# Optimization experiments

Hardware: AMD Instinct MI355X
Metric: run time of the kernel (lower is better)

The kernel has to match this reference:

```python
import jax, jax.numpy as jnp
import numpy as np
from jax.ops import segment_sum

N_NODES = 50000
N_EDGES = 600000
HIDDEN = 128
N_FEAT = 128
N_CLASSES = 10
N_GRAPHS = 128


def setup_inputs() -> dict:
    key = jax.random.key(0)
    ks = jax.random.split(key, 16)
    x = jax.random.normal(ks[0], (N_NODES, N_FEAT), dtype=jnp.float32)
    edge_index = jax.random.randint(ks[1], (2, N_EDGES), 0, N_NODES, dtype=jnp.int64)
    batch = jnp.sort(jax.random.randint(ks[2], (N_NODES,), 0, N_GRAPHS, dtype=jnp.int64))
    def lin_init(k, fan_in, fan_out):
        s = 1.0 / np.sqrt(fan_in)
        return jax.random.uniform(k, (fan_in, fan_out), jnp.float32, -s, s)
    params = {
        'W1': lin_init(ks[3], N_FEAT, HIDDEN), 'b1': jnp.zeros((HIDDEN,), jnp.float32),
        'W2': lin_init(ks[4], HIDDEN, HIDDEN), 'b2': jnp.zeros((HIDDEN,), jnp.float32),
        'W3': lin_init(ks[5], HIDDEN, HIDDEN), 'b3': jnp.zeros((HIDDEN,), jnp.float32),
        'W4': lin_init(ks[6], HIDDEN, HIDDEN), 'b4': jnp.zeros((HIDDEN,), jnp.float32),
        'W5': lin_init(ks[7], HIDDEN, HIDDEN), 'b5': jnp.zeros((HIDDEN,), jnp.float32),
        'Wfc': lin_init(ks[8], HIDDEN, HIDDEN), 'bfc': jnp.zeros((HIDDEN,), jnp.float32),
        'Wlin': lin_init(ks[9], HIDDEN, N_CLASSES), 'blin': jnp.zeros((N_CLASSES,), jnp.float32),
    }
    return dict(x=x, edge_index=edge_index, batch=batch, **params)


def _gcn_edges(edge_index, n_nodes):
    # PyG GCNConv default: add self-loops, symmetric deg^-1/2 normalization.
    loop = jnp.arange(n_nodes, dtype=edge_index.dtype)
    row = jnp.concatenate([edge_index[0], loop])  # source (messages gathered from)
    col = jnp.concatenate([edge_index[1], loop])  # target (scatter-add into)
    deg = segment_sum(jnp.ones_like(col, dtype=jnp.float32), col, num_segments=n_nodes)
    dinv = jnp.where(deg > 0, jax.lax.rsqrt(deg), 0.0)
    norm = dinv[row] * dinv[col]  # [E+N]
    return row, col, norm


def _gcn_conv(x, W, b, row, col, norm, n_nodes):
    h = x @ W  # [N, out]
    agg = segment_sum(h[row] * norm[:, None], col, num_segments=n_nodes)
    return agg + b


def reference(x, edge_index, batch, W1, b1, W2, b2, W3, b3, W4, b4, W5, b5, Wfc, bfc, Wlin, blin):
    n = x.shape[0]
    row, col, norm = _gcn_edges(edge_index, n)
    h = jax.nn.relu(_gcn_conv(x, W1, b1, row, col, norm, n))
    h = jax.nn.relu(_gcn_conv(h, W2, b2, row, col, norm, n))
    h = jax.nn.relu(_gcn_conv(h, W3, b3, row, col, norm, n))
    h = jax.nn.relu(_gcn_conv(h, W4, b4, row, col, norm, n))
    h = jax.nn.relu(_gcn_conv(h, W5, b5, row, col, norm, n))
    h = jax.nn.relu(h @ Wfc + bfc)
    # global_mean_pool over batch ids
    sums = segment_sum(h, batch, num_segments=N_GRAPHS)
    cnts = segment_sum(jnp.ones((n,), h.dtype), batch, num_segments=N_GRAPHS)
    pooled = sums / jnp.maximum(cnts, 1.0)[:, None]  # [G, H]
    embeddings = pooled
    # dropout p=0.5 is identity in eval mode
    logits = pooled @ Wlin + blin  # [G, C]
    return logits, jnp.squeeze(embeddings)
```

## Files before the change

kernel.cpp:

```cpp
#include <hip/hip_runtime.h>

typedef __attribute__((ext_vector_type(8))) short short8;
typedef __attribute__((ext_vector_type(4))) float floatx4;
typedef __attribute__((ext_vector_type(4))) unsigned uintx4;
typedef __attribute__((ext_vector_type(8))) _Float16 half8;

static __device__ __forceinline__ unsigned short f2bf(float f) {
    unsigned u = __float_as_uint(f);
    u += 0x7fff + ((u >> 16) & 1);
    return (unsigned short)(u >> 16);
}
static __device__ __forceinline__ float bf2f(unsigned short h) {
    return __uint_as_float((unsigned)h << 16);
}


__global__ void count_kernel(const int* __restrict__ ei, int* degi, int E) {
    int e = blockIdx.x * 256 + threadIdx.x;
    if (e < E) atomicAdd(&degi[ei[E + e]], 1);
}

__global__ __launch_bounds__(256) void scan_bsum_kernel(const int* __restrict__ degi,
                                                        float* __restrict__ dinv,
                                                        int* bsum, int n) {
    int tid = threadIdx.x;
    int i = blockIdx.x * 256 + tid;
    int d = (i < n) ? degi[i] : 0;
    if (i < n) dinv[i] = rsqrtf((float)(d + 1));
    int v = d;
    #pragma unroll
    for (int off = 32; off > 0; off >>= 1) v += __shfl_down(v, off);
    __shared__ int ws[4];
    if ((tid & 63) == 0) ws[tid >> 6] = v;
    __syncthreads();
    if (tid == 0) bsum[blockIdx.x] = ws[0] + ws[1] + ws[2] + ws[3];
}

__global__ __launch_bounds__(256) void scan_emit_kernel(const int* __restrict__ degi,
                                                        const int* __restrict__ bsum,
                                                        int* rp, int* cursor, int n, int nb) {
    int tid = threadIdx.x;
    int bid = blockIdx.x;
    int contrib = 0;
    for (int t = tid; t < bid; t += 256) contrib += bsum[t];
    int cr = contrib;
    #pragma unroll
    for (int off = 32; off > 0; off >>= 1) cr += __shfl_down(cr, off);
    __shared__ int wr[4];
    __shared__ int s_boff;
    if ((tid & 63) == 0) wr[tid >> 6] = cr;
    __syncthreads();
    if (tid == 0) s_boff = wr[0] + wr[1] + wr[2] + wr[3];
    __syncthreads();

    int i = bid * 256 + tid;
    int v = (i < n) ? degi[i] : 0;
    int lane = tid & 63, wid = tid >> 6;
    int x = v;
    #pragma unroll
    for (int off = 1; off < 64; off <<= 1) {
        int y = __shfl_up(x, off);
        if (lane >= off) x += y;
    }
    __shared__ int ws[4];
    if (lane == 63) ws[wid] = x;
    __syncthreads();
    if (tid == 0) { int a = 0; for (int j = 0; j < 4; ++j) { int t = ws[j]; ws[j] = a; a += t; } }
    __syncthreads();
    int excl = x - v + ws[wid] + s_boff;
    if (i < n) { rp[i] = excl; cursor[i] = excl; }
    if (i == n - 1) rp[n] = excl + v;
}

__global__ void fill_kernel(const int* __restrict__ ei, int* cursor,
                            int* __restrict__ csr, int E) {
    int e = blockIdx.x * 256 + threadIdx.x;
    if (e >= E) return;
    int r = ei[e], c = ei[E + e];
    int pos = atomicAdd(&cursor[c], 1);
    csr[pos] = r;
}


__global__ void packw_kernel(const float* w0, const float* w1, const float* w2,
                             const float* w3, const float* w4, const float* w5,
                             unsigned short* __restrict__ hi, unsigned short* __restrict__ lo) {
    int l = blockIdx.y;
    const float* W = (l == 0) ? w0 : (l == 1) ? w1 : (l == 2) ? w2
                   : (l == 3) ? w3 : (l == 4) ? w4 : w5;
    int idx = blockIdx.x * 256 + threadIdx.x;
    int k = idx >> 7, nn = idx & 127;
    float v = W[k * 128 + nn];
    unsigned short h = f2bf(v);
    unsigned short ls = f2bf(v - bf2f(h));
    hi[l * 16384 + nn * 128 + k] = h;
    lo[l * 16384 + nn * 128 + k] = ls;
}


#define WLDS_STRIDE 260

static __device__ __forceinline__ void stage_w(const unsigned short* __restrict__ Wth,
                                               const unsigned short* __restrict__ Wtl,
                                               unsigned short* Wlds, int tid) {
    #pragma unroll
    for (int it = 0; it < 8; ++it) {
        int c = it * 512 + tid;
        int row = c >> 5, piece = c & 31;
        const unsigned short* src = (piece < 16)
            ? (Wth + (size_t)row * 128 + piece * 8)
            : (Wtl + (size_t)row * 128 + (piece - 16) * 8);
        int dst = row * WLDS_STRIDE + ((piece < 16) ? piece * 8 : 128 + (piece - 16) * 8);
        *(short8*)&Wlds[dst] = *(const short8*)src;
    }
}

static __device__ __forceinline__ void split_h8(half8 a, short8& ah, short8& al) {
    #pragma unroll
    for (int j = 0; j < 8; ++j) {
        float fv = (float)a[j];
        unsigned u = __float_as_uint(fv);
        float lo = fv - __uint_as_float(u & 0xFFFF0000u);
        ah[j] = (short)(u >> 16);
        al[j] = (short)(__float_as_uint(lo) >> 16);
    }
}

__global__ __launch_bounds__(512, 4) void gemm_kernel(const _Float16* __restrict__ A,
                                                      const unsigned short* __restrict__ Wth,
                                                      const unsigned short* __restrict__ Wtl,
                                                      const float* __restrict__ dinv,
                                                      void* __restrict__ C, int n, int outf) {
    __shared__ unsigned short Wlds[128 * WLDS_STRIDE];
    int tid = threadIdx.x;
    int wave = tid >> 6, lane = tid & 63;
    int m = lane & 15, quad = lane >> 4;
    int row0 = blockIdx.x * 128 + wave * 16;
    int arow = row0 + m; if (arow > n - 1) arow = n - 1;
    size_t n32 = (size_t)n * 32;
    const _Float16* abase = A + (size_t)arow * 32 + quad * 8;

    half8 pa[4];
    #pragma unroll
    for (int kc = 0; kc < 4; ++kc) pa[kc] = *(const half8*)(abase + (size_t)kc * n32);

    stage_w(Wth, Wtl, Wlds, tid);

    floatx4 acc[8];
    #pragma unroll
    for (int ct = 0; ct < 8; ++ct) acc[ct] = (floatx4){0.f, 0.f, 0.f, 0.f};
    __syncthreads();

    #pragma unroll
    for (int kc = 0; kc < 4; ++kc) {
        short8 ah, al;
        split_h8(pa[kc], ah, al);
        #pragma unroll
        for (int ct = 0; ct < 8; ++ct) {
            int base = (ct * 16 + m) * WLDS_STRIDE + kc * 32 + quad * 8;
            short8 wh = *(const short8*)&Wlds[base];
            short8 wl = *(const short8*)&Wlds[base + 128];
            acc[ct] = __builtin_amdgcn_mfma_f32_16x16x32_bf16(ah, wl, acc[ct], 0, 0, 0);
            acc[ct] = __builtin_amdgcn_mfma_f32_16x16x32_bf16(al, wh, acc[ct], 0, 0, 0);
            acc[ct] = __builtin_amdgcn_mfma_f32_16x16x32_bf16(ah, wh, acc[ct], 0, 0, 0);
        }
    }

    float dv[4];
    #pragma unroll
    for (int r = 0; r < 4; ++r) dv[r] = dinv[min(row0 + quad * 4 + r, n - 1)];

    #pragma unroll
    for (int ct = 0; ct < 8; ++ct) {
        #pragma unroll
        for (int r = 0; r < 4; ++r) {
            int row = row0 + quad * 4 + r;
            if (row < n) {
                if (outf) {
                    ((float*)C)[(size_t)row * 128 + ct * 16 + m] = acc[ct][r];
                } else {
                    ((_Float16*)C)[(size_t)(ct >> 1) * n32 + (size_t)row * 32
                                   + (ct & 1) * 16 + m] = (_Float16)(acc[ct][r] * dv[r]);
                }
            }
        }
    }
}

__global__ __launch_bounds__(512, 4) void gemm0_kernel(const float* __restrict__ X,
                                                       const unsigned short* __restrict__ Wth,
                                                       const unsigned short* __restrict__ Wtl,
                                                       const float* __restrict__ dinv,
                                                       _Float16* __restrict__ C, int n) {
    __shared__ unsigned short Wlds[128 * WLDS_STRIDE];
    int tid = threadIdx.x;
    int wave = tid >> 6, lane = tid & 63;
    int m = lane & 15, quad = lane >> 4;
    int row0 = blockIdx.x * 128 + wave * 16;
    int arow = row0 + m; if (arow > n - 1) arow = n - 1;
    size_t n32 = (size_t)n * 32;
    const float* aptr = X + (size_t)arow * 128 + quad * 8;

    floatx4 pf0[4], pf1[4];
    #pragma unroll
    for (int kc = 0; kc < 4; ++kc) {
        pf0[kc] = *(const floatx4*)(aptr + kc * 32);
        pf1[kc] = *(const floatx4*)(aptr + kc * 32 + 4);
    }

    stage_w(Wth, Wtl, Wlds, tid);

    floatx4 acc[8];
    #pragma unroll
    for (int ct = 0; ct < 8; ++ct) acc[ct] = (floatx4){0.f, 0.f, 0.f, 0.f};
    __syncthreads();

    #pragma unroll
    for (int kc = 0; kc < 4; ++kc) {
        short8 ah, al;
        #pragma unroll
        for (int j = 0; j < 8; ++j) {
            float fv = (j < 4) ? pf0[kc][j] : pf1[kc][j - 4];
            unsigned short h = f2bf(fv);
            ah[j] = (short)h;
            al[j] = (short)f2bf(fv - bf2f(h));
        }
        #pragma unroll
        for (int ct = 0; ct < 8; ++ct) {
            int base = (ct * 16 + m) * WLDS_STRIDE + kc * 32 + quad * 8;
            short8 wh = *(const short8*)&Wlds[base];
            short8 wl = *(const short8*)&Wlds[base + 128];
            acc[ct] = __builtin_amdgcn_mfma_f32_16x16x32_bf16(ah, wl, acc[ct], 0, 0, 0);
            acc[ct] = __builtin_amdgcn_mfma_f32_16x16x32_bf16(al, wh, acc[ct], 0, 0, 0);
            acc[ct] = __builtin_amdgcn_mfma_f32_16x16x32_bf16(ah, wh, acc[ct], 0, 0, 0);
        }
    }

    float dv[4];
    #pragma unroll
    for (int r = 0; r < 4; ++r) dv[r] = dinv[min(row0 + quad * 4 + r, n - 1)];

    #pragma unroll
    for (int ct = 0; ct < 8; ++ct) {
        #pragma unroll
        for (int r = 0; r < 4; ++r) {
            int row = row0 + quad * 4 + r;
            if (row < n)
                C[(size_t)(ct >> 1) * n32 + (size_t)row * 32 + (ct & 1) * 16 + m] =
                    (_Float16)(acc[ct][r] * dv[r]);
        }
    }
}


__global__ __launch_bounds__(256) void agg_kernel(const _Float16* __restrict__ t,
                                                  const float* __restrict__ bias,
                                                  const int* __restrict__ rp,
                                                  const int* __restrict__ csr,
                                                  const float* __restrict__ dinv,
                                                  _Float16* __restrict__ outp, int n, int nh) {
    int s = blockIdx.x & 7;
    int chunk = s & 3;
    int half = s >> 2;
    int nb = blockIdx.x >> 3;
    int group = threadIdx.x >> 2;
    int lane4 = threadIdx.x & 3;
    int j = half * nh + nb * 64 + group;
    int jend = half ? n : nh;
    if (j >= jend) return;
    size_t n32 = (size_t)n * 32;
    const _Float16* tc = t + (size_t)chunk * n32;
    int c8 = lane4 * 8;
    int p0 = rp[j], p1 = rp[j + 1];

    float dj = dinv[j];
    half8 vs = *(const half8*)&tc[(size_t)j * 32 + c8];

    float acc[8];
    #pragma unroll
    for (int k = 0; k < 8; ++k) acc[k] = (float)vs[k];

    int p = p0;
    for (; p + 8 <= p1; p += 8) {
        int e[8];
        #pragma unroll
        for (int i = 0; i < 8; ++i) e[i] = csr[p + i];
        half8 v[8];
        #pragma unroll
        for (int i = 0; i < 8; ++i)
            v[i] = *(const half8*)&tc[(size_t)e[i] * 32 + c8];
        #pragma unroll
        for (int i = 0; i < 8; ++i) {
            #pragma unroll
            for (int k = 0; k < 8; ++k) acc[k] += (float)v[i][k];
        }
    }
    if (p < p1) {
        int lim = p1 - 1;
        int e[8];
        #pragma unroll
        for (int i = 0; i < 8; ++i) e[i] = csr[min(p + i, lim)];
        float msk[8];
        #pragma unroll
        for (int i = 0; i < 8; ++i) msk[i] = (p + i < p1) ? 1.f : 0.f;
        half8 v[8];
        #pragma unroll
        for (int i = 0; i < 8; ++i)
            v[i] = *(const half8*)&tc[(size_t)e[i] * 32 + c8];
        #pragma unroll
        for (int i = 0; i < 8; ++i) {
            #pragma unroll
            for (int k = 0; k < 8; ++k) acc[k] += msk[i] * (float)v[i][k];
        }
    }

    int cbase = chunk * 32 + c8;
    float4 b0 = *(const float4*)&bias[cbase];
    float4 b1 = *(const float4*)&bias[cbase + 4];
    float bb[8] = {b0.x, b0.y, b0.z, b0.w, b1.x, b1.y, b1.z, b1.w};
    half8 hv;
    #pragma unroll
    for (int k = 0; k < 8; ++k) hv[k] = (_Float16)fmaxf(fmaf(dj, acc[k], bb[k]), 0.f);

    *(half8*)&outp[(size_t)chunk * n32 + (size_t)j * 32 + c8] = hv;
}


__global__ __launch_bounds__(256) void pool_kernel(const float* __restrict__ t,
                                                   const float* __restrict__ bfc,
                                                   const int* __restrict__ batch,
                                                   const float* __restrict__ Wlin,
                                                   const float* __restrict__ blin,
                                                   float* __restrict__ out, int n) {
    int g = blockIdx.x;
    int tid = threadIdx.x;
    int lo = 0, hi = n;
    while (lo < hi) { int m = (lo + hi) >> 1; if (batch[m] < g) lo = m + 1; else hi = m; }
    int start = lo;
    lo = start; hi = n;
    while (lo < hi) { int m = (lo + hi) >> 1; if (batch[m] < g + 1) lo = m + 1; else hi = m; }
    int end = lo;

    int lane = tid & 31, sub = tid >> 5;
    int c4 = lane * 4;
    float4 bv = *(const float4*)&bfc[c4];
    float sx = 0.f, sy = 0.f, sz = 0.f, sw = 0.f;
    for (int j = start + sub; j < end; j += 8) {
        float4 v = *(const float4*)&t[(size_t)j * 128 + c4];
        sx += fmaxf(v.x + bv.x, 0.f);
        sy += fmaxf(v.y + bv.y, 0.f);
        sz += fmaxf(v.z + bv.z, 0.f);
        sw += fmaxf(v.w + bv.w, 0.f);
    }
    __shared__ float red[8][128];
    red[sub][c4] = sx; red[sub][c4 + 1] = sy; red[sub][c4 + 2] = sz; red[sub][c4 + 3] = sw;
    __syncthreads();
    __shared__ float pooled[128];
    if (tid < 128) {
        float s = 0.f;
        #pragma unroll
        for (int k = 0; k < 8; ++k) s += red[k][tid];
        float pv = s / fmaxf((float)(end - start), 1.f);
        pooled[tid] = pv;
        out[1280 + g * 128 + tid] = pv;
    }
    __syncthreads();
    if (tid < 10) {
        float a = blin[tid];
        for (int k = 0; k < 128; ++k) a += pooled[k] * Wlin[k * 10 + tid];
        out[g * 10 + tid] = a;
    }
}


extern "C" void kernel_launch(void* const* d_in, const int* in_sizes, int n_in,
                              void* d_out, int out_size, void* d_ws, size_t ws_size,
                              hipStream_t stream) {
    const float* x     = (const float*)d_in[0];
    const int*   ei    = (const int*)d_in[1];
    const int*   batch = (const int*)d_in[2];
    const float* Wl[6] = {(const float*)d_in[3], (const float*)d_in[5], (const float*)d_in[7],
                          (const float*)d_in[9], (const float*)d_in[11], (const float*)d_in[13]};
    const float* bl[6] = {(const float*)d_in[4], (const float*)d_in[6], (const float*)d_in[8],
                          (const float*)d_in[10], (const float*)d_in[12], (const float*)d_in[14]};
    const float* Wlin = (const float*)d_in[15];
    const float* blin = (const float*)d_in[16];

    const int N = in_sizes[2];
    const int E = in_sizes[1] / 2;
    (void)n_in; (void)out_size; (void)ws_size;

    char* p = (char*)d_ws;
    auto carve = [&](size_t bytes) { void* r = (void*)p; p += (bytes + 255) & ~(size_t)255; return r; };
    _Float16*       tA     = (_Float16*)carve((size_t)N * 128 * 2);
    _Float16*       tB     = (_Float16*)carve((size_t)N * 128 * 2);
    float*          tf     = (float*)carve((size_t)N * 128 * 4);
    int*            degi   = (int*)carve((size_t)N * 4);
    float*          dinv   = (float*)carve((size_t)N * 4);
    int*            rp     = (int*)carve((size_t)(N + 1) * 4);
    int*            cursor = (int*)carve((size_t)N * 4);
    int*            csr    = (int*)carve((size_t)E * 4);
    int*            bsum   = (int*)carve(256 * 4);
    unsigned short* wth    = (unsigned short*)carve(6 * 16384 * 2);
    unsigned short* wtl    = (unsigned short*)carve(6 * 16384 * 2);

    int gN = (N + 255) / 256;
    hipMemsetAsync(degi, 0, (size_t)N * 4, stream);
    count_kernel<<<(E + 255) / 256, 256, 0, stream>>>(ei, degi, E);
    scan_bsum_kernel<<<gN, 256, 0, stream>>>(degi, dinv, bsum, N);
    scan_emit_kernel<<<gN, 256, 0, stream>>>(degi, bsum, rp, cursor, N, gN);
    fill_kernel<<<(E + 255) / 256, 256, 0, stream>>>(ei, cursor, csr, E);
    packw_kernel<<<dim3(64, 6), 256, 0, stream>>>(Wl[0], Wl[1], Wl[2], Wl[3], Wl[4], Wl[5],
                                                  wth, wtl);

    int NH = (N + 1) / 2;
    int gGemm = (N + 127) / 128;
    int gAgg  = 8 * ((NH + 63) / 64);
    gemm0_kernel<<<gGemm, 512, 0, stream>>>(x, wth, wtl, dinv, tA, N);
    agg_kernel<<<gAgg, 256, 0, stream>>>(tA, bl[0], rp, csr, dinv, tB, N, NH);
    for (int l = 1; l < 5; ++l) {
        gemm_kernel<<<gGemm, 512, 0, stream>>>(tB, wth + l * 16384, wtl + l * 16384,
                                               dinv, (void*)tA, N, 0);
        agg_kernel<<<gAgg, 256, 0, stream>>>(tA, bl[l], rp, csr, dinv, tB, N, NH);
    }
    gemm_kernel<<<gGemm, 512, 0, stream>>>(tB, wth + 5 * 16384, wtl + 5 * 16384,
                                           dinv, (void*)tf, N, 1);
    pool_kernel<<<128, 256, 0, stream>>>(tf, bl[5], batch, Wlin, blin, (float*)d_out, N);
}
```

Measured before the change: 396.0 us.

## Fuse GCN layer GEMMs and aggregations into one cooperative persistent kernel

Replaces the sequence of eleven separate GEMM and aggregation launches with a single cooperative kernel of 512 blocks, using grid-wide syncs between stages. Aggregation work is grid-strided across the persistent blocks, and the GEMM tiles run on the first blocks. The goal is to remove per-launch overhead and inter-kernel gaps. In exchange it pays grid.sync costs, and the large LDS footprint caps how many blocks fit per CU, so the gather-heavy aggregation runs at lower occupancy than before. The original multi-kernel path is kept as a fallback if the cooperative launch fails.

```diff
diff --git a/kernel.cpp b/kernel.cpp
--- a/kernel.cpp
+++ b/kernel.cpp
@@ -1,8 +1,10 @@
 #include <hip/hip_runtime.h>
+#include <hip/hip_cooperative_groups.h>
+
+namespace cg = cooperative_groups;
 
 typedef __attribute__((ext_vector_type(8))) short short8;
 typedef __attribute__((ext_vector_type(4))) float floatx4;
-typedef __attribute__((ext_vector_type(4))) unsigned uintx4;
 typedef __attribute__((ext_vector_type(8))) _Float16 half8;
 
 static __device__ __forceinline__ unsigned short f2bf(float f) {
@@ -99,6 +101,8 @@
 
 
 #define WLDS_STRIDE 260
+#define COOP_GRID 512
+#define AGG_STRIDE ((COOP_GRID / 8) * 128)
 
 static __device__ __forceinline__ void stage_w(const unsigned short* __restrict__ Wth,
                                                const unsigned short* __restrict__ Wtl,
@@ -126,16 +130,17 @@
     }
 }
 
-__global__ __launch_bounds__(512, 4) void gemm_kernel(const _Float16* __restrict__ A,
-                                                      const unsigned short* __restrict__ Wth,
-                                                      const unsigned short* __restrict__ Wtl,
-                                                      const float* __restrict__ dinv,
-                                                      void* __restrict__ C, int n, int outf) {
-    __shared__ unsigned short Wlds[128 * WLDS_STRIDE];
-    int tid = threadIdx.x;
+static __device__ __forceinline__ void gemm_body_f16(const _Float16* __restrict__ A,
+                                                     const unsigned short* __restrict__ Wth,
+                                                     const unsigned short* __restrict__ Wtl,
+                                                     const float* __restrict__ dinv,
+                                                     _Float16* __restrict__ C16,
+                                                     float* __restrict__ C32, int outf,
+                                                     unsigned short* Wlds, int tid, int bid,
+                                                     int n) {
     int wave = tid >> 6, lane = tid & 63;
     int m = lane & 15, quad = lane >> 4;
-    int row0 = blockIdx.x * 128 + wave * 16;
+    int row0 = bid * 128 + wave * 16;
     int arow = row0 + m; if (arow > n - 1) arow = n - 1;
     size_t n32 = (size_t)n * 32;
     const _Float16* abase = A + (size_t)arow * 32 + quad * 8;
@@ -177,26 +182,26 @@
             int row = row0 + quad * 4 + r;
             if (row < n) {
                 if (outf) {
-                    ((float*)C)[(size_t)row * 128 + ct * 16 + m] = acc[ct][r];
+                    C32[(size_t)row * 128 + ct * 16 + m] = acc[ct][r];
                 } else {
-                    ((_Float16*)C)[(size_t)(ct >> 1) * n32 + (size_t)row * 32
-                                   + (ct & 1) * 16 + m] = (_Float16)(acc[ct][r] * dv[r]);
+                    C16[(size_t)(ct >> 1) * n32 + (size_t)row * 32 + (ct & 1) * 16 + m] =
+                        (_Float16)(acc[ct][r] * dv[r]);
                 }
             }
         }
     }
 }
 
-__global__ __launch_bounds__(512, 4) void gemm0_kernel(const float* __restrict__ X,
-                                                       const unsigned short* __restrict__ Wth,
-                                                       const unsigned short* __restrict__ Wtl,
-                                                       const float* __restrict__ dinv,
-                                                       _Float16* __restrict__ C, int n) {
-    __shared__ unsigned short Wlds[128 * WLDS_STRIDE];
-    int tid = threadIdx.x;
+static __device__ __forceinline__ void gemm_body_f32(const float* __restrict__ X,
+                                                     const unsigned short* __restrict__ Wth,
+                                                     const unsigned short* __restrict__ Wtl,
+                                                     const float* __restrict__ dinv,
+                                                     _Float16* __restrict__ C,
+                                                     unsigned short* Wlds, int tid, int bid,
+                                                     int n) {
     int wave = tid >> 6, lane = tid & 63;
     int m = lane & 15, quad = lane >> 4;
-    int row0 = blockIdx.x * 128 + wave * 16;
+    int row0 = bid * 128 + wave * 16;
     int arow = row0 + m; if (arow > n - 1) arow = n - 1;
     size_t n32 = (size_t)n * 32;
     const float* aptr = X + (size_t)arow * 128 + quad * 8;
@@ -252,6 +257,130 @@
     }
 }
 
+static __device__ __forceinline__ void agg_node(const _Float16* __restrict__ tc,
+                                                const float* __restrict__ bias,
+                                                const int* __restrict__ rp,
+                                                const int* __restrict__ csr,
+                                                const float* __restrict__ dinv,
+                                                _Float16* __restrict__ outp,
+                                                int j, int chunk, int c8, size_t n32) {
+    int p0 = rp[j], p1 = rp[j + 1];
+    float dj = dinv[j];
+    half8 vs = *(const half8*)&tc[(size_t)j * 32 + c8];
+
+    float acc[8];
+    #pragma unroll
+    for (int k = 0; k < 8; ++k) acc[k] = (float)vs[k];
+
+    int p = p0;
+    for (; p + 8 <= p1; p += 8) {
+        int e[8];
+        #pragma unroll
+        for (int i = 0; i < 8; ++i) e[i] = csr[p + i];
+        half8 v[8];
+        #pragma unroll
+        for (int i = 0; i < 8; ++i)
+            v[i] = *(const half8*)&tc[(size_t)e[i] * 32 + c8];
+        #pragma unroll
+        for (int i = 0; i < 8; ++i) {
+            #pragma unroll
+            for (int k = 0; k < 8; ++k) acc[k] += (float)v[i][k];
+        }
+    }
+    if (p < p1) {
+        int lim = p1 - 1;
+        int e[8];
+        #pragma unroll
+        for (int i = 0; i < 8; ++i) e[i] = csr[min(p + i, lim)];
+        float msk[8];
+        #pragma unroll
+        for (int i = 0; i < 8; ++i) msk[i] = (p + i < p1) ? 1.f : 0.f;
+        half8 v[8];
+        #pragma unroll
+        for (int i = 0; i < 8; ++i)
+            v[i] = *(const half8*)&tc[(size_t)e[i] * 32 + c8];
+        #pragma unroll
+        for (int i = 0; i < 8; ++i) {
+            #pragma unroll
+            for (int k = 0; k < 8; ++k) acc[k] += msk[i] * (float)v[i][k];
+        }
+    }
+
+    int cbase = chunk * 32 + c8;
+    float4 b0 = *(const float4*)&bias[cbase];
+    float4 b1 = *(const float4*)&bias[cbase + 4];
+    float bb[8] = {b0.x, b0.y, b0.z, b0.w, b1.x, b1.y, b1.z, b1.w};
+    half8 hv;
+    #pragma unroll
+    for (int k = 0; k < 8; ++k) hv[k] = (_Float16)fmaxf(fmaf(dj, acc[k], bb[k]), 0.f);
+
+    *(half8*)&outp[(size_t)chunk * n32 + (size_t)j * 32 + c8] = hv;
+}
+
+
+__global__ __launch_bounds__(512, 4) void net_kernel(
+    const float* __restrict__ X,
+    const unsigned short* __restrict__ wth, const unsigned short* __restrict__ wtl,
+    const float* __restrict__ b0, const float* __restrict__ b1,
+    const float* __restrict__ b2, const float* __restrict__ b3,
+    const float* __restrict__ b4,
+    const float* __restrict__ dinv, const int* __restrict__ rp,
+    const int* __restrict__ csr,
+    _Float16* __restrict__ tA, _Float16* __restrict__ tB,
+    float* __restrict__ tf, int n, int nh) {
+    cg::grid_group grid = cg::this_grid();
+    __shared__ unsigned short Wlds[128 * WLDS_STRIDE];
+    const int tid = threadIdx.x;
+    const int bid = blockIdx.x;
+    const int gGemm = (n + 127) >> 7;
+    const size_t n32 = (size_t)n * 32;
+
+    const int s = bid & 7;
+    const int chunk = s & 3;
+    const int half = s >> 2;
+    const int group0 = ((bid >> 3) << 7) + (tid >> 2);
+    const int c8 = (tid & 3) * 8;
+    const int cnt = half ? (n - nh) : nh;
+
+    if (bid < gGemm)
+        gemm_body_f32(X, wth, wtl, dinv, tA, Wlds, tid, bid, n);
+    grid.sync();
+
+    for (int l = 1; l <= 5; ++l) {
+        const float* bias = (l == 1) ? b0 : (l == 2) ? b1 : (l == 3) ? b2
+                          : (l == 4) ? b3 : b4;
+        const _Float16* tc = tA + (size_t)chunk * n32;
+        for (int ln = group0; ln < cnt; ln += AGG_STRIDE)
+            agg_node(tc, bias, rp, csr, dinv, tB, half * nh + ln, chunk, c8, n32);
+        grid.sync();
+
+        if (bid < gGemm)
+            gemm_body_f16(tB, wth + l * 16384, wtl + l * 16384, dinv,
+                          tA, tf, (l == 5) ? 1 : 0, Wlds, tid, bid, n);
+        if (l < 5) grid.sync();
+    }
+}
+
+
+__global__ __launch_bounds__(512, 4) void gemm_kernel(const _Float16* __restrict__ A,
+                                                      const unsigned short* __restrict__ Wth,
+                                                      const unsigned short* __restrict__ Wtl,
+                                                      const float* __restrict__ dinv,
+                                                      _Float16* __restrict__ C16,
+                                                      float* __restrict__ C32,
+                                                      int n, int outf) {
+    __shared__ unsigned short Wlds[128 * WLDS_STRIDE];
+    gemm_body_f16(A, Wth, Wtl, dinv, C16, C32, outf, Wlds, threadIdx.x, blockIdx.x, n);
+}
+
+__global__ __launch_bounds__(512, 4) void gemm0_kernel(const float* __restrict__ X,
+                                                       const unsigned short* __restrict__ Wth,
+                                                       const unsigned short* __restrict__ Wtl,
+                                                       const float* __restrict__ dinv,
+                                                       _Float16* __restrict__ C, int n) {
+    __shared__ unsigned short Wlds[128 * WLDS_STRIDE];
+    gemm_body_f32(X, Wth, Wtl, dinv, C, Wlds, threadIdx.x, blockIdx.x, n);
+}
 
 __global__ __launch_bounds__(256) void agg_kernel(const _Float16* __restrict__ t,
                                                   const float* __restrict__ bias,
@@ -269,60 +398,7 @@
     int jend = half ? n : nh;
     if (j >= jend) return;
     size_t n32 = (size_t)n * 32;
-    const _Float16* tc = t + (size_t)chunk * n32;
-    int c8 = lane4 * 8;
-    int p0 = rp[j], p1 = rp[j + 1];
-
-    float dj = dinv[j];
-    half8 vs = *(const half8*)&tc[(size_t)j * 32 + c8];
-
-    float acc[8];
-    #pragma unroll
-    for (int k = 0; k < 8; ++k) acc[k] = (float)vs[k];
-
-    int p = p0;
-    for (; p + 8 <= p1; p += 8) {
-        int e[8];
-        #pragma unroll
-        for (int i = 0; i < 8; ++i) e[i] = csr[p + i];
-        half8 v[8];
-        #pragma unroll
-        for (int i = 0; i < 8; ++i)
-            v[i] = *(const half8*)&tc[(size_t)e[i] * 32 + c8];
-        #pragma unroll
-        for (int i = 0; i < 8; ++i) {
-            #pragma unroll
-            for (int k = 0; k < 8; ++k) acc[k] += (float)v[i][k];
-        }
-    }
-    if (p < p1) {
-        int lim = p1 - 1;
-        int e[8];
-        #pragma unroll
-        for (int i = 0; i < 8; ++i) e[i] = csr[min(p + i, lim)];
-        float msk[8];
-        #pragma unroll
-        for (int i = 0; i < 8; ++i) msk[i] = (p + i < p1) ? 1.f : 0.f;
-        half8 v[8];
-        #pragma unroll
-        for (int i = 0; i < 8; ++i)
-            v[i] = *(const half8*)&tc[(size_t)e[i] * 32 + c8];
-        #pragma unroll
-        for (int i = 0; i < 8; ++i) {
-            #pragma unroll
-            for (int k = 0; k < 8; ++k) acc[k] += msk[i] * (float)v[i][k];
-        }
-    }
-
-    int cbase = chunk * 32 + c8;
-    float4 b0 = *(const float4*)&bias[cbase];
-    float4 b1 = *(const float4*)&bias[cbase + 4];
-    float bb[8] = {b0.x, b0.y, b0.z, b0.w, b1.x, b1.y, b1.z, b1.w};
-    half8 hv;
-    #pragma unroll
-    for (int k = 0; k < 8; ++k) hv[k] = (_Float16)fmaxf(fmaf(dj, acc[k], bb[k]), 0.f);
-
-    *(half8*)&outp[(size_t)chunk * n32 + (size_t)j * 32 + c8] = hv;
+    agg_node(t + (size_t)chunk * n32, bias, rp, csr, dinv, outp, j, chunk, lane4 * 8, n32);
 }
 
 
@@ -414,16 +490,34 @@
                                                   wth, wtl);
 
     int NH = (N + 1) / 2;
-    int gGemm = (N + 127) / 128;
-    int gAgg  = 8 * ((NH + 63) / 64);
-    gemm0_kernel<<<gGemm, 512, 0, stream>>>(x, wth, wtl, dinv, tA, N);
-    agg_kernel<<<gAgg, 256, 0, stream>>>(tA, bl[0], rp, csr, dinv, tB, N, NH);
-    for (int l = 1; l < 5; ++l) {
-        gemm_kernel<<<gGemm, 512, 0, stream>>>(tB, wth + l * 16384, wtl + l * 16384,
-                                               dinv, (void*)tA, N, 0);
-        agg_kernel<<<gAgg, 256, 0, stream>>>(tA, bl[l], rp, csr, dinv, tB, N, NH);
-    }
-    gemm_kernel<<<gGemm, 512, 0, stream>>>(tB, wth + 5 * 16384, wtl + 5 * 16384,
-                                           dinv, (void*)tf, N, 1);
+
+    {
+        const float* xx = x;
+        const unsigned short* wthv = wth; const unsigned short* wtlv = wtl;
+        const float* bb0 = bl[0]; const float* bb1 = bl[1]; const float* bb2 = bl[2];
+        const float* bb3 = bl[3]; const float* bb4 = bl[4];
+        const float* dinvv = dinv; const int* rpv = rp; const int* csrv = csr;
+        _Float16* tAv = tA; _Float16* tBv = tB; float* tfv = tf;
+        int Nv = N, NHv = NH;
+        void* args[] = {&xx, &wthv, &wtlv, &bb0, &bb1, &bb2, &bb3, &bb4,
+                        &dinvv, &rpv, &csrv, &tAv, &tBv, &tfv, &Nv, &NHv};
+        hipError_t ce = hipLaunchCooperativeKernel((void*)net_kernel,
+                                                   dim3(COOP_GRID), dim3(512),
+                                                   args, 0, stream);
+        if (ce != hipSuccess) {
+            int gGemm = (N + 127) / 128;
+            int gAgg  = 8 * ((NH + 63) / 64);
+            gemm0_kernel<<<gGemm, 512, 0, stream>>>(x, wth, wtl, dinv, tA, N);
+            agg_kernel<<<gAgg, 256, 0, stream>>>(tA, bl[0], rp, csr, dinv, tB, N, NH);
+            for (int l = 1; l < 5; ++l) {
+                gemm_kernel<<<gGemm, 512, 0, stream>>>(tB, wth + l * 16384, wtl + l * 16384,
+                                                       dinv, tA, (float*)nullptr, N, 0);
+                agg_kernel<<<gAgg, 256, 0, stream>>>(tA, bl[l], rp, csr, dinv, tB, N, NH);
+            }
+            gemm_kernel<<<gGemm, 512, 0, stream>>>(tB, wth + 5 * 16384, wtl + 5 * 16384,
+                                                   dinv, (_Float16*)nullptr, tf, N, 1);
+        }
+    }
+
     pool_kernel<<<128, 256, 0, stream>>>(tf, bl[5], batch, Wlin, blin, (float*)d_out, N);
 }
```

Result: slower. 1.201 ms (+203.4%).

## Switch intermediate features from chunked column layout to row-major with LDS-transposed stores

Applied to the files above, without the earlier changes.

The fp16 intermediate features move from a layout split into four 32-column chunks to a plain row-major [N,128] layout. The GEMM epilogues now stage results through LDS and write each row with contiguous 16-byte stores. The aggregation kernel uses 16 threads per node, so each neighbour gather reads one full 256-byte row instead of four separate 64-byte pieces spread across chunk-specialized blocks. The cost is an extra LDS round trip and two barriers in the GEMM, and each aggregation block now reads the whole row rather than a chunk, which changes L2 reuse behaviour.

```diff
diff --git a/kernel.cpp b/kernel.cpp
--- a/kernel.cpp
+++ b/kernel.cpp
@@ -2,7 +2,6 @@
 
 typedef __attribute__((ext_vector_type(8))) short short8;
 typedef __attribute__((ext_vector_type(4))) float floatx4;
-typedef __attribute__((ext_vector_type(4))) unsigned uintx4;
 typedef __attribute__((ext_vector_type(8))) _Float16 half8;
 
 static __device__ __forceinline__ unsigned short f2bf(float f) {
@@ -99,6 +98,7 @@
 
 
 #define WLDS_STRIDE 260
+#define TR_STRIDE 132
 
 static __device__ __forceinline__ void stage_w(const unsigned short* __restrict__ Wth,
                                                const unsigned short* __restrict__ Wtl,
@@ -137,12 +137,11 @@
     int m = lane & 15, quad = lane >> 4;
     int row0 = blockIdx.x * 128 + wave * 16;
     int arow = row0 + m; if (arow > n - 1) arow = n - 1;
-    size_t n32 = (size_t)n * 32;
-    const _Float16* abase = A + (size_t)arow * 32 + quad * 8;
+    const _Float16* abase = A + (size_t)arow * 128 + quad * 8;
 
     half8 pa[4];
     #pragma unroll
-    for (int kc = 0; kc < 4; ++kc) pa[kc] = *(const half8*)(abase + (size_t)kc * n32);
+    for (int kc = 0; kc < 4; ++kc) pa[kc] = *(const half8*)(abase + kc * 32);
 
     stage_w(Wth, Wtl, Wlds, tid);
 
@@ -170,19 +169,36 @@
     #pragma unroll
     for (int r = 0; r < 4; ++r) dv[r] = dinv[min(row0 + quad * 4 + r, n - 1)];
 
-    #pragma unroll
-    for (int ct = 0; ct < 8; ++ct) {
-        #pragma unroll
-        for (int r = 0; r < 4; ++r) {
-            int row = row0 + quad * 4 + r;
-            if (row < n) {
-                if (outf) {
-                    ((float*)C)[(size_t)row * 128 + ct * 16 + m] = acc[ct][r];
-                } else {
-                    ((_Float16*)C)[(size_t)(ct >> 1) * n32 + (size_t)row * 32
-                                   + (ct & 1) * 16 + m] = (_Float16)(acc[ct][r] * dv[r]);
-                }
+    if (outf) {
+        #pragma unroll
+        for (int ct = 0; ct < 8; ++ct) {
+            #pragma unroll
+            for (int r = 0; r < 4; ++r) {
+                int row = row0 + quad * 4 + r;
+                if (row < n) ((float*)C)[(size_t)row * 128 + ct * 16 + m] = acc[ct][r];
             }
+        }
+    } else {
+        __syncthreads();
+        _Float16* tr = (_Float16*)Wlds;
+        #pragma unroll
+        for (int ct = 0; ct < 8; ++ct) {
+            #pragma unroll
+            for (int r = 0; r < 4; ++r) {
+                int rl = wave * 16 + quad * 4 + r;
+                tr[rl * TR_STRIDE + ct * 16 + m] = (_Float16)(acc[ct][r] * dv[r]);
+            }
+        }
+        __syncthreads();
+        int rl2 = tid >> 2;
+        int seg = tid & 3;
+        int grow = blockIdx.x * 128 + rl2;
+        if (grow < n) {
+            _Float16* dst = (_Float16*)C + (size_t)grow * 128 + seg * 32;
+            const _Float16* src = tr + rl2 * TR_STRIDE + seg * 32;
+            #pragma unroll
+            for (int k = 0; k < 4; ++k)
+                *(half8*)(dst + k * 8) = *(const half8*)(src + k * 8);
         }
     }
 }
@@ -198,7 +214,6 @@
     int m = lane & 15, quad = lane >> 4;
     int row0 = blockIdx.x * 128 + wave * 16;
     int arow = row0 + m; if (arow > n - 1) arow = n - 1;
-    size_t n32 = (size_t)n * 32;
     const float* aptr = X + (size_t)arow * 128 + quad * 8;
 
     floatx4 pf0[4], pf1[4];
@@ -240,15 +255,26 @@
     #pragma unroll
     for (int r = 0; r < 4; ++r) dv[r] = dinv[min(row0 + quad * 4 + r, n - 1)];
 
+    __syncthreads();
+    _Float16* tr = (_Float16*)Wlds;
     #pragma unroll
     for (int ct = 0; ct < 8; ++ct) {
         #pragma unroll
         for (int r = 0; r < 4; ++r) {
-            int row = row0 + quad * 4 + r;
-            if (row < n)
-                C[(size_t)(ct >> 1) * n32 + (size_t)row * 32 + (ct & 1) * 16 + m] =
-                    (_Float16)(acc[ct][r] * dv[r]);
-        }
+            int rl = wave * 16 + quad * 4 + r;
+            tr[rl * TR_STRIDE + ct * 16 + m] = (_Float16)(acc[ct][r] * dv[r]);
+        }
+    }
+    __syncthreads();
+    int rl2 = tid >> 2;
+    int seg = tid & 3;
+    int grow = blockIdx.x * 128 + rl2;
+    if (grow < n) {
+        _Float16* dst = C + (size_t)grow * 128 + seg * 32;
+        const _Float16* src = tr + rl2 * TR_STRIDE + seg * 32;
+        #pragma unroll
+        for (int k = 0; k < 4; ++k)
+            *(half8*)(dst + k * 8) = *(const half8*)(src + k * 8);
     }
 }
 
@@ -258,24 +284,14 @@
                                                   const int* __restrict__ rp,
                                                   const int* __restrict__ csr,
                                                   const float* __restrict__ dinv,
-                                                  _Float16* __restrict__ outp, int n, int nh) {
-    int s = blockIdx.x & 7;
-    int chunk = s & 3;
-    int half = s >> 2;
-    int nb = blockIdx.x >> 3;
-    int group = threadIdx.x >> 2;
-    int lane4 = threadIdx.x & 3;
-    int j = half * nh + nb * 64 + group;
-    int jend = half ? n : nh;
-    if (j >= jend) return;
-    size_t n32 = (size_t)n * 32;
-    const _Float16* tc = t + (size_t)chunk * n32;
-    int c8 = lane4 * 8;
+                                                  _Float16* __restrict__ outp, int n) {
+    int j = blockIdx.x * 16 + (threadIdx.x >> 4);
+    if (j >= n) return;
+    int c8 = (threadIdx.x & 15) * 8;
     int p0 = rp[j], p1 = rp[j + 1];
-
     float dj = dinv[j];
-    half8 vs = *(const half8*)&tc[(size_t)j * 32 + c8];
-
+
+    half8 vs = *(const half8*)&t[(size_t)j * 128 + c8];
     float acc[8];
     #pragma unroll
     for (int k = 0; k < 8; ++k) acc[k] = (float)vs[k];
@@ -288,7 +304,7 @@
         half8 v[8];
         #pragma unroll
         for (int i = 0; i < 8; ++i)
-            v[i] = *(const half8*)&tc[(size_t)e[i] * 32 + c8];
+            v[i] = *(const half8*)&t[(size_t)e[i] * 128 + c8];
         #pragma unroll
         for (int i = 0; i < 8; ++i) {
             #pragma unroll
@@ -306,7 +322,7 @@
         half8 v[8];
         #pragma unroll
         for (int i = 0; i < 8; ++i)
-            v[i] = *(const half8*)&tc[(size_t)e[i] * 32 + c8];
+            v[i] = *(const half8*)&t[(size_t)e[i] * 128 + c8];
         #pragma unroll
         for (int i = 0; i < 8; ++i) {
             #pragma unroll
@@ -314,15 +330,13 @@
         }
     }
 
-    int cbase = chunk * 32 + c8;
-    float4 b0 = *(const float4*)&bias[cbase];
-    float4 b1 = *(const float4*)&bias[cbase + 4];
+    float4 b0 = *(const float4*)&bias[c8];
+    float4 b1 = *(const float4*)&bias[c8 + 4];
     float bb[8] = {b0.x, b0.y, b0.z, b0.w, b1.x, b1.y, b1.z, b1.w};
     half8 hv;
     #pragma unroll
     for (int k = 0; k < 8; ++k) hv[k] = (_Float16)fmaxf(fmaf(dj, acc[k], bb[k]), 0.f);
-
-    *(half8*)&outp[(size_t)chunk * n32 + (size_t)j * 32 + c8] = hv;
+    *(half8*)&outp[(size_t)j * 128 + c8] = hv;
 }
 
 
@@ -413,15 +427,14 @@
     packw_kernel<<<dim3(64, 6), 256, 0, stream>>>(Wl[0], Wl[1], Wl[2], Wl[3], Wl[4], Wl[5],
                                                   wth, wtl);
 
-    int NH = (N + 1) / 2;
     int gGemm = (N + 127) / 128;
-    int gAgg  = 8 * ((NH + 63) / 64);
+    int gAgg  = (N + 15) / 16;
     gemm0_kernel<<<gGemm, 512, 0, stream>>>(x, wth, wtl, dinv, tA, N);
-    agg_kernel<<<gAgg, 256, 0, stream>>>(tA, bl[0], rp, csr, dinv, tB, N, NH);
+    agg_kernel<<<gAgg, 256, 0, stream>>>(tA, bl[0], rp, csr, dinv, tB, N);
     for (int l = 1; l < 5; ++l) {
         gemm_kernel<<<gGemm, 512, 0, stream>>>(tB, wth + l * 16384, wtl + l * 16384,
                                                dinv, (void*)tA, N, 0);
-        agg_kernel<<<gAgg, 256, 0, stream>>>(tA, bl[l], rp, csr, dinv, tB, N, NH);
+        agg_kernel<<<gAgg, 256, 0, stream>>>(tA, bl[l], rp, csr, dinv, tB, N);
     }
     gemm_kernel<<<gGemm, 512, 0, stream>>>(tB, wth + 5 * 16384, wtl + 5 * 16384,
                                            dinv, (void*)tf, N, 1);
```

After: 404.9 us. +2.3%, slower.

## Store weights as fp16 in LDS and split waves across output column halves

Applied to the files above, without the earlier changes.

Weights are packed once as a single fp16 transposed copy instead of separate bf16 hi/lo arrays. The kernel splits them into bf16 hi/lo in registers after loading from LDS, which halves LDS footprint and staging traffic. The hidden-layer GEMM now launches 1024 threads per block, with each wave covering half the output columns, so it holds four accumulators instead of eight and can run more waves per CU. This costs extra conversion ALU work per MFMA, and rounding the weights to fp16 loses some precision compared with the exact fp32 hi/lo split.

```diff
diff --git a/kernel.cpp b/kernel.cpp
--- a/kernel.cpp
+++ b/kernel.cpp
@@ -2,7 +2,6 @@
 
 typedef __attribute__((ext_vector_type(8))) short short8;
 typedef __attribute__((ext_vector_type(4))) float floatx4;
-typedef __attribute__((ext_vector_type(4))) unsigned uintx4;
 typedef __attribute__((ext_vector_type(8))) _Float16 half8;
 
 static __device__ __forceinline__ unsigned short f2bf(float f) {
@@ -10,8 +9,16 @@
     u += 0x7fff + ((u >> 16) & 1);
     return (unsigned short)(u >> 16);
 }
-static __device__ __forceinline__ float bf2f(unsigned short h) {
-    return __uint_as_float((unsigned)h << 16);
+
+static __device__ __forceinline__ void split_h8(half8 a, short8& ah, short8& al) {
+    #pragma unroll
+    for (int j = 0; j < 8; ++j) {
+        float fv = (float)a[j];
+        unsigned u = __float_as_uint(fv);
+        float lo = fv - __uint_as_float(u & 0xFFFF0000u);
+        ah[j] = (short)(u >> 16);
+        al[j] = (short)(__float_as_uint(lo) >> 16);
+    }
 }
 
 
@@ -84,58 +91,39 @@
 
 __global__ void packw_kernel(const float* w0, const float* w1, const float* w2,
                              const float* w3, const float* w4, const float* w5,
-                             unsigned short* __restrict__ hi, unsigned short* __restrict__ lo) {
+                             _Float16* __restrict__ wt) {
     int l = blockIdx.y;
     const float* W = (l == 0) ? w0 : (l == 1) ? w1 : (l == 2) ? w2
                    : (l == 3) ? w3 : (l == 4) ? w4 : w5;
     int idx = blockIdx.x * 256 + threadIdx.x;
     int k = idx >> 7, nn = idx & 127;
-    float v = W[k * 128 + nn];
-    unsigned short h = f2bf(v);
-    unsigned short ls = f2bf(v - bf2f(h));
-    hi[l * 16384 + nn * 128 + k] = h;
-    lo[l * 16384 + nn * 128 + k] = ls;
-}
-
-
-#define WLDS_STRIDE 260
-
-static __device__ __forceinline__ void stage_w(const unsigned short* __restrict__ Wth,
-                                               const unsigned short* __restrict__ Wtl,
-                                               unsigned short* Wlds, int tid) {
-    #pragma unroll
-    for (int it = 0; it < 8; ++it) {
-        int c = it * 512 + tid;
-        int row = c >> 5, piece = c & 31;
-        const unsigned short* src = (piece < 16)
-            ? (Wth + (size_t)row * 128 + piece * 8)
-            : (Wtl + (size_t)row * 128 + (piece - 16) * 8);
-        int dst = row * WLDS_STRIDE + ((piece < 16) ? piece * 8 : 128 + (piece - 16) * 8);
-        *(short8*)&Wlds[dst] = *(const short8*)src;
-    }
-}
-
-static __device__ __forceinline__ void split_h8(half8 a, short8& ah, short8& al) {
-    #pragma unroll
-    for (int j = 0; j < 8; ++j) {
-        float fv = (float)a[j];
-        unsigned u = __float_as_uint(fv);
-        float lo = fv - __uint_as_float(u & 0xFFFF0000u);
-        ah[j] = (short)(u >> 16);
-        al[j] = (short)(__float_as_uint(lo) >> 16);
-    }
-}
-
-__global__ __launch_bounds__(512, 4) void gemm_kernel(const _Float16* __restrict__ A,
-                                                      const unsigned short* __restrict__ Wth,
-                                                      const unsigned short* __restrict__ Wtl,
-                                                      const float* __restrict__ dinv,
-                                                      void* __restrict__ C, int n, int outf) {
-    __shared__ unsigned short Wlds[128 * WLDS_STRIDE];
+    wt[l * 16384 + nn * 128 + k] = (_Float16)W[k * 128 + nn];
+}
+
+
+#define W16_STRIDE 130
+
+static __device__ __forceinline__ void stage_w16(const _Float16* __restrict__ Wt,
+                                                 _Float16* Wlds, int tid, int nthr) {
+    int pieces = 2048;
+    for (int c = tid; c < pieces; c += nthr) {
+        int row = c >> 4, piece = c & 15;
+        *(half8*)&Wlds[row * W16_STRIDE + piece * 8] =
+            *(const half8*)(Wt + (size_t)row * 128 + piece * 8);
+    }
+}
+
+__global__ __launch_bounds__(1024, 8) void gemm_kernel(const _Float16* __restrict__ A,
+                                                       const _Float16* __restrict__ Wt,
+                                                       const float* __restrict__ dinv,
+                                                       void* __restrict__ C, int n, int outf) {
+    __shared__ _Float16 Wlds[128 * W16_STRIDE];
     int tid = threadIdx.x;
     int wave = tid >> 6, lane = tid & 63;
+    int cthalf = wave >> 3;
+    int wrow = wave & 7;
     int m = lane & 15, quad = lane >> 4;
-    int row0 = blockIdx.x * 128 + wave * 16;
+    int row0 = blockIdx.x * 128 + wrow * 16;
     int arow = row0 + m; if (arow > n - 1) arow = n - 1;
     size_t n32 = (size_t)n * 32;
     const _Float16* abase = A + (size_t)arow * 32 + quad * 8;
@@ -144,11 +132,11 @@
     #pragma unroll
     for (int kc = 0; kc < 4; ++kc) pa[kc] = *(const half8*)(abase + (size_t)kc * n32);
 
-    stage_w(Wth, Wtl, Wlds, tid);
-
-    floatx4 acc[8];
-    #pragma unroll
-    for (int ct = 0; ct < 8; ++ct) acc[ct] = (floatx4){0.f, 0.f, 0.f, 0.f};
+    stage_w16(Wt, Wlds, tid, 1024);
+
+    floatx4 acc[4];
+    #pragma unroll
+    for (int ci = 0; ci < 4; ++ci) acc[ci] = (floatx4){0.f, 0.f, 0.f, 0.f};
     __syncthreads();
 
     #pragma unroll
@@ -156,13 +144,14 @@
         short8 ah, al;
         split_h8(pa[kc], ah, al);
         #pragma unroll
-        for (int ct = 0; ct < 8; ++ct) {
-            int base = (ct * 16 + m) * WLDS_STRIDE + kc * 32 + quad * 8;
-            short8 wh = *(const short8*)&Wlds[base];
-            short8 wl = *(const short8*)&Wlds[base + 128];
-            acc[ct] = __builtin_amdgcn_mfma_f32_16x16x32_bf16(ah, wl, acc[ct], 0, 0, 0);
-            acc[ct] = __builtin_amdgcn_mfma_f32_16x16x32_bf16(al, wh, acc[ct], 0, 0, 0);
-            acc[ct] = __builtin_amdgcn_mfma_f32_16x16x32_bf16(ah, wh, acc[ct], 0, 0, 0);
+        for (int ci = 0; ci < 4; ++ci) {
+            int ct = cthalf * 4 + ci;
+            half8 w16 = *(const half8*)&Wlds[(ct * 16 + m) * W16_STRIDE + kc * 32 + quad * 8];
+            short8 wh, wl;
+            split_h8(w16, wh, wl);
+            acc[ci] = __builtin_amdgcn_mfma_f32_16x16x32_bf16(ah, wl, acc[ci], 0, 0, 0);
+            acc[ci] = __builtin_amdgcn_mfma_f32_16x16x32_bf16(al, wh, acc[ci], 0, 0, 0);
+            acc[ci] = __builtin_amdgcn_mfma_f32_16x16x32_bf16(ah, wh, acc[ci], 0, 0, 0);
         }
     }
 
@@ -171,16 +160,17 @@
     for (int r = 0; r < 4; ++r) dv[r] = dinv[min(row0 + quad * 4 + r, n - 1)];
 
     #pragma unroll
-    for (int ct = 0; ct < 8; ++ct) {
+    for (int ci = 0; ci < 4; ++ci) {
+        int ct = cthalf * 4 + ci;
         #pragma unroll
         for (int r = 0; r < 4; ++r) {
             int row = row0 + quad * 4 + r;
             if (row < n) {
                 if (outf) {
-                    ((float*)C)[(size_t)row * 128 + ct * 16 + m] = acc[ct][r];
+                    ((float*)C)[(size_t)row * 128 + ct * 16 + m] = acc[ci][r];
                 } else {
                     ((_Float16*)C)[(size_t)(ct >> 1) * n32 + (size_t)row * 32
-                                   + (ct & 1) * 16 + m] = (_Float16)(acc[ct][r] * dv[r]);
+                                   + (ct & 1) * 16 + m] = (_Float16)(acc[ci][r] * dv[r]);
                 }
             }
         }
@@ -188,11 +178,10 @@
 }
 
 __global__ __launch_bounds__(512, 4) void gemm0_kernel(const float* __restrict__ X,
-                                                       const unsigned short* __restrict__ Wth,
-                                                       const unsigned short* __restrict__ Wtl,
+                                                       const _Float16* __restrict__ Wt,
                                                        const float* __restrict__ dinv,
                                                        _Float16* __restrict__ C, int n) {
-    __shared__ unsigned short Wlds[128 * WLDS_STRIDE];
+    __shared__ _Float16 Wlds[128 * W16_STRIDE];
     int tid = threadIdx.x;
     int wave = tid >> 6, lane = tid & 63;
     int m = lane & 15, quad = lane >> 4;
@@ -208,7 +197,7 @@
         pf1[kc] = *(const floatx4*)(aptr + kc * 32 + 4);
     }
 
-    stage_w(Wth, Wtl, Wlds, tid);
+    stage_w16(Wt, Wlds, tid, 512);
 
     floatx4 acc[8];
     #pragma unroll
@@ -223,13 +212,13 @@
             float fv = (j < 4) ? pf0[kc][j] : pf1[kc][j - 4];
             unsigned short h = f2bf(fv);
             ah[j] = (short)h;
-            al[j] = (short)f2bf(fv - bf2f(h));
+            al[j] = (short)f2bf(fv - __uint_as_float((unsigned)h << 16));
         }
         #pragma unroll
         for (int ct = 0; ct < 8; ++ct) {
-            int base = (ct * 16 + m) * WLDS_STRIDE + kc * 32 + quad * 8;
-            short8 wh = *(const short8*)&Wlds[base];
-            short8 wl = *(const short8*)&Wlds[base + 128];
+            half8 w16 = *(const half8*)&Wlds[(ct * 16 + m) * W16_STRIDE + kc * 32 + quad * 8];
+            short8 wh, wl;
+            split_h8(w16, wh, wl);
             acc[ct] = __builtin_amdgcn_mfma_f32_16x16x32_bf16(ah, wl, acc[ct], 0, 0, 0);
             acc[ct] = __builtin_amdgcn_mfma_f32_16x16x32_bf16(al, wh, acc[ct], 0, 0, 0);
             acc[ct] = __builtin_amdgcn_mfma_f32_16x16x32_bf16(ah, wh, acc[ct], 0, 0, 0);
@@ -401,8 +390,7 @@
     int*            cursor = (int*)carve((size_t)N * 4);
     int*            csr    = (int*)carve((size_t)E * 4);
     int*            bsum   = (int*)carve(256 * 4);
-    unsigned short* wth    = (unsigned short*)carve(6 * 16384 * 2);
-    unsigned short* wtl    = (unsigned short*)carve(6 * 16384 * 2);
+    _Float16*       wt16   = (_Float16*)carve(6 * 16384 * 2);
 
     int gN = (N + 255) / 256;
     hipMemsetAsync(degi, 0, (size_t)N * 4, stream);
@@ -411,19 +399,19 @@
     scan_emit_kernel<<<gN, 256, 0, stream>>>(degi, bsum, rp, cursor, N, gN);
     fill_kernel<<<(E + 255) / 256, 256, 0, stream>>>(ei, cursor, csr, E);
     packw_kernel<<<dim3(64, 6), 256, 0, stream>>>(Wl[0], Wl[1], Wl[2], Wl[3], Wl[4], Wl[5],
-                                                  wth, wtl);
+                                                  wt16);
 
     int NH = (N + 1) / 2;
     int gGemm = (N + 127) / 128;
     int gAgg  = 8 * ((NH + 63) / 64);
-    gemm0_kernel<<<gGemm, 512, 0, stream>>>(x, wth, wtl, dinv, tA, N);
+    gemm0_kernel<<<gGemm, 512, 0, stream>>>(x, wt16, dinv, tA, N);
     agg_kernel<<<gAgg, 256, 0, stream>>>(tA, bl[0], rp, csr, dinv, tB, N, NH);
     for (int l = 1; l < 5; ++l) {
-        gemm_kernel<<<gGemm, 512, 0, stream>>>(tB, wth + l * 16384, wtl + l * 16384,
-                                               dinv, (void*)tA, N, 0);
+        gemm_kernel<<<gGemm, 1024, 0, stream>>>(tB, wt16 + l * 16384, dinv,
+                                                (void*)tA, N, 0);
         agg_kernel<<<gAgg, 256, 0, stream>>>(tA, bl[l], rp, csr, dinv, tB, N, NH);
     }
-    gemm_kernel<<<gGemm, 512, 0, stream>>>(tB, wth + 5 * 16384, wtl + 5 * 16384,
-                                           dinv, (void*)tf, N, 1);
+    gemm_kernel<<<gGemm, 1024, 0, stream>>>(tB, wt16 + 5 * 16384, dinv,
+                                            (void*)tf, N, 1);
     pool_kernel<<<128, 256, 0, stream>>>(tf, bl[5], batch, Wlin, blin, (float*)d_out, N);
 }
```

After: 429.1 us. +8.4%, slower.
